# Optimization experiments

Measured on AMD Instinct MI355X. Metric: run time of the kernel, lower is better.

## Reference

```python
import jax, jax.numpy as jnp
import numpy as np

D_MODEL = 768
HEAD = 12
D_K = D_MODEL // HEAD


def setup_inputs() -> dict:
    key = jax.random.key(0)
    ks = jax.random.split(key, 9)
    s = 1.0 / np.sqrt(D_MODEL)
    return {
        "x": jax.random.normal(ks[0], (2, 4096, D_MODEL), dtype=jnp.float32),
        "Wq": jax.random.normal(ks[1], (D_MODEL, D_MODEL), dtype=jnp.float32) * s,
        "bq": jax.random.normal(ks[2], (D_MODEL,), dtype=jnp.float32) * 0.01,
        "Wk": jax.random.normal(ks[3], (D_MODEL, D_MODEL), dtype=jnp.float32) * s,
        "bk": jax.random.normal(ks[4], (D_MODEL,), dtype=jnp.float32) * 0.01,
        "Wv": jax.random.normal(ks[5], (D_MODEL, D_MODEL), dtype=jnp.float32) * s,
        "bv": jax.random.normal(ks[6], (D_MODEL,), dtype=jnp.float32) * 0.01,
        "Wo": jax.random.normal(ks[7], (D_MODEL, D_MODEL), dtype=jnp.float32) * s,
        "bo": jax.random.normal(ks[8], (D_MODEL,), dtype=jnp.float32) * 0.01,
    }


def reference(x, Wq, bq, Wk, bk, Wv, bv, Wo, bo):
    B, S, _ = x.shape
    # Linear projections, split into heads: [B, H, S, d_k]
    def proj(W, b):
        return (x @ W + b).reshape(B, S, HEAD, D_K).transpose(0, 2, 1, 3)
    Q, K, V = proj(Wq, bq), proj(Wk, bk), proj(Wv, bv)
    scale = 1.0 / jnp.sqrt(jnp.asarray(D_K, x.dtype))
    # [B, H, S, S] attention scores (materialized, as in the original module)
    scores = jnp.einsum('bhqd,bhkd->bhqk', Q, K) * scale
    probs = jax.nn.softmax(scores, axis=-1)  # dropout is identity in eval mode
    ctx = jnp.einsum('bhqk,bhkd->bhqd', probs, V)
    ctx = ctx.transpose(0, 2, 1, 3).reshape(B, S, D_MODEL)
    return ctx @ Wo + bo
```

## Files before the change

### kernel.cpp

```cpp
#include <hip/hip_runtime.h>

#define D_MODEL 768
#define S_LEN   4096
#define NHEAD   12
#define DK      64
#define TKA     64

typedef _Float16 f16;
typedef _Float16 f16x8 __attribute__((ext_vector_type(8)));
typedef _Float16 f16x4 __attribute__((ext_vector_type(4)));
typedef __fp16   fp16x2 __attribute__((ext_vector_type(2)));
typedef float    f32x4 __attribute__((ext_vector_type(4)));
typedef float    f32x2 __attribute__((ext_vector_type(2)));

#define MFMA16(a, b, c) __builtin_amdgcn_mfma_f32_16x16x32_f16(a, b, c, 0, 0, 0)

#define Q_PRESCALE 0.18033688f
#define SOFTMAX_C  11.54156036f

__device__ inline f16x8 ldf(const f16* p) {
    return *reinterpret_cast<const f16x8*>(p);
}

__device__ inline void gl2lds16(const f16* g, f16* l) {
    __builtin_amdgcn_global_load_lds(
        (const __attribute__((address_space(1))) void*)g,
        (__attribute__((address_space(3))) void*)l, 16, 0, 0);
}

__global__ __launch_bounds__(256) void cvt_x_kernel(const float* __restrict__ x,
                                                    f16* __restrict__ xb) {
    size_t i = ((size_t)blockIdx.x * 256 + threadIdx.x) * 4;
    float4 v = *reinterpret_cast<const float4*>(x + i);
    f16x4 o = { (f16)v.x, (f16)v.y, (f16)v.z, (f16)v.w };
    *reinterpret_cast<f16x4*>(xb + i) = o;
}

__global__ __launch_bounds__(256) void wtrans_kernel(const float* __restrict__ Wq,
                                                     const float* __restrict__ Wk,
                                                     const float* __restrict__ Wv,
                                                     const float* __restrict__ Wo,
                                                     f16* __restrict__ WT) {
    const int z = blockIdx.z;
    const float* in = (z == 0) ? Wq : (z == 1) ? Wk : (z == 2) ? Wv : Wo;
    f16* out = WT + (size_t)z * D_MODEL * D_MODEL;
    __shared__ float tile[32][33];
    const int tx = threadIdx.x, ty = threadIdx.y;
    const int n0 = blockIdx.x * 32, k0 = blockIdx.y * 32;
#pragma unroll
    for (int j = 0; j < 32; j += 8)
        tile[ty + j][tx] = in[(size_t)(k0 + ty + j) * D_MODEL + n0 + tx];
    __syncthreads();
#pragma unroll
    for (int j = 0; j < 32; j += 8)
        out[(size_t)(n0 + ty + j) * D_MODEL + k0 + tx] = (f16)tile[tx][ty + j];
}

__global__ __launch_bounds__(256, 3) void gemm_qkv_kernel(
        const f16* __restrict__ A, const f16* __restrict__ WT,
        const float* __restrict__ bq, const float* __restrict__ bk,
        const float* __restrict__ bv,
        f16* __restrict__ Qb, f16* __restrict__ Kb, f16* __restrict__ Vt) {
    __shared__ __align__(16) f16 asmem[3][128 * 32];
    __shared__ __align__(16) f16 bsmem[3][128 * 32];
    const int z = blockIdx.z;
    const f16* Bt = WT + (size_t)z * D_MODEL * D_MODEL;
    const float* bias = (z == 0) ? bq : (z == 1) ? bk : bv;
    const int w = threadIdx.x >> 6;
    const int lane = threadIdx.x & 63;
    const int ln = lane & 15, quad = lane >> 4;
    const int mb = blockIdx.x * 128;
    const int nb = blockIdx.y * 128;
    const int mloc = (w & 1) * 64, nloc = (w >> 1) * 64;
    const int l0 = w * 64 + lane;

    auto stage = [&](int buf, int kb) {
#pragma unroll
        for (int p = 0; p < 2; p++) {
            const int l = p * 256 + l0;
            gl2lds16(A + (size_t)(mb + (l >> 2)) * D_MODEL + kb + (l & 3) * 8,
                     &asmem[buf][(p * 256 + w * 64) * 8]);
        }
#pragma unroll
        for (int p = 0; p < 2; p++) {
            const int l = p * 256 + l0;
            gl2lds16(Bt + (size_t)(nb + (l >> 2)) * D_MODEL + kb + (l & 3) * 8,
                     &bsmem[buf][(p * 256 + w * 64) * 8]);
        }
    };

    f32x4 acc[4][4] = {};
    stage(0, 0);
    stage(1, 32);
    __syncthreads();

    const int NIT = D_MODEL / 32;
    int cb = 0, sb = 2;
    for (int it = 0; it < NIT; ++it) {
        f16x8 af[4], bf[4];
#pragma unroll
        for (int i = 0; i < 4; i++)
            af[i] = ldf(&asmem[cb][(mloc + i * 16 + ln) * 32 + quad * 8]);
#pragma unroll
        for (int t = 0; t < 4; t++)
            bf[t] = ldf(&bsmem[cb][(nloc + t * 16 + ln) * 32 + quad * 8]);
#pragma unroll
        for (int i = 0; i < 4; i++)
#pragma unroll
            for (int t = 0; t < 4; t++)
                acc[i][t] = MFMA16(af[i], bf[t], acc[i][t]);
        __syncthreads();
        if (it + 2 < NIT) stage(sb, (it + 2) * 32);
        cb = (cb == 2) ? 0 : cb + 1;
        sb = (sb == 2) ? 0 : sb + 1;
    }

#pragma unroll
    for (int t = 0; t < 4; t++) {
        const int n = nb + nloc + t * 16 + ln;
        const float bval = bias[n];
        const int h = n >> 6, d = n & 63;
#pragma unroll
        for (int i = 0; i < 4; i++) {
            const int m = mb + mloc + i * 16 + quad * 4;
            const int b = m >> 12, s = m & 4095;
            const int bh = b * NHEAD + h;
            if (z == 0) {
#pragma unroll
                for (int r = 0; r < 4; r++)
                    Qb[((size_t)bh * S_LEN + s + r) * DK + d] =
                        (f16)((acc[i][t][r] + bval) * Q_PRESCALE);
            } else if (z == 1) {
#pragma unroll
                for (int r = 0; r < 4; r++)
                    Kb[((size_t)bh * S_LEN + s + r) * DK + d] =
                        (f16)(acc[i][t][r] + bval);
            } else {
                f16x4 pk;
#pragma unroll
                for (int r = 0; r < 4; r++) pk[r] = (f16)(acc[i][t][r] + bval);
                *reinterpret_cast<f16x4*>(&Vt[((size_t)bh * DK + d) * S_LEN + s]) = pk;
            }
        }
    }
}

__global__ __launch_bounds__(256, 3) void attn_kernel(const f16* __restrict__ Qb,
                                                      const f16* __restrict__ Kb,
                                                      const f16* __restrict__ Vt,
                                                      f16* __restrict__ Ctx) {
    __shared__ __align__(16) f16 kbuf[3][TKA * DK];
    __shared__ __align__(16) f16 vbuf[3][DK * TKA];

    const int w = threadIdx.x >> 6;
    const int lane = threadIdx.x & 63;
    const int ln = lane & 15, quad = lane >> 4;

    const int blk = blockIdx.x;
    const int xcd = blk & 7, sidx = blk >> 3;
    const int bh = xcd * 3 + (sidx >> 5);
    const int qb = (sidx & 31) * 128;
    const int b = bh / NHEAD, h = bh % NHEAD;

    const f16* Kbh = Kb + (size_t)bh * S_LEN * DK;
    const f16* Vbh = Vt + (size_t)bh * DK * S_LEN;

    f16x8 aq[2][2];
#pragma unroll
    for (int i2 = 0; i2 < 2; i2++) {
        const f16* qp = Qb + ((size_t)bh * S_LEN + qb + w * 32 + i2 * 16 + ln) * DK;
        aq[i2][0] = ldf(qp + quad * 8);
        aq[i2][1] = ldf(qp + 32 + quad * 8);
    }

    int rS[2], ckS[2], cvS[2];
#pragma unroll
    for (int p = 0; p < 2; p++) {
        const int l = p * 256 + w * 64 + lane;
        const int r = l >> 3;
        rS[p]  = r;
        ckS[p] = ((l & 7) - r - (r >> 2)) & 7;
        cvS[p] = ((l & 7) - r - (r >> 3)) & 7;
    }

    auto stage = [&](int buf, int kk) {
#pragma unroll
        for (int p = 0; p < 2; p++)
            gl2lds16(Kbh + (size_t)(kk + rS[p]) * DK + ckS[p] * 8,
                     &kbuf[buf][(p * 256 + w * 64) * 8]);
#pragma unroll
        for (int p = 0; p < 2; p++)
            gl2lds16(Vbh + (size_t)rS[p] * S_LEN + kk + cvS[p] * 8,
                     &vbuf[buf][(p * 256 + w * 64) * 8]);
    };

    int koff[2][2][2];
#pragma unroll
    for (int kt = 0; kt < 2; kt++)
#pragma unroll
        for (int a = 0; a < 2; a++) {
            const int rr = kt * 32 + 8 * (ln >> 2) + 4 * a + (ln & 3);
            const int sw = rr + (rr >> 2);
            koff[kt][a][0] = rr * DK + (((quad + sw) & 7) * 8);
            koff[kt][a][1] = rr * DK + (((quad + 4 + sw) & 7) * 8);
        }
    int voff[4][2];
#pragma unroll
    for (int t = 0; t < 4; t++) {
        const int rr = t * 16 + ln;
        const int sw = rr + (rr >> 3);
#pragma unroll
        for (int kt = 0; kt < 2; kt++)
            voff[t][kt] = rr * TKA + (((quad + 4 * kt + sw) & 7) * 8);
    }

    const f32x4 cinit = { -SOFTMAX_C, -SOFTMAX_C, -SOFTMAX_C, -SOFTMAX_C };
    f32x4 acc[4][2] = {};
    f32x2 lsum2[2] = {};

    stage(0, 0);
    stage(1, TKA);
    __syncthreads();

    const int NIT = S_LEN / TKA;
    int cb = 0, sb = 2;
    for (int it = 0; it < NIT; ++it) {
        const f16* kb = kbuf[cb];
        const f16* vb = vbuf[cb];

        union { f16x8 v; fp16x2 h2[4]; } pb[2][2];

#pragma unroll
        for (int kt = 0; kt < 2; kt++) {
#pragma unroll
            for (int a = 0; a < 2; a++) {
                const f16x8 kf0 = ldf(kb + koff[kt][a][0]);
                const f16x8 kf1 = ldf(kb + koff[kt][a][1]);
#pragma unroll
                for (int i2 = 0; i2 < 2; i2++) {
                    f32x4 si = MFMA16(kf0, aq[i2][0], cinit);
                    si = MFMA16(kf1, aq[i2][1], si);
                    const float e0 = __builtin_amdgcn_exp2f(si[0]);
                    const float e1 = __builtin_amdgcn_exp2f(si[1]);
                    const float e2 = __builtin_amdgcn_exp2f(si[2]);
                    const float e3 = __builtin_amdgcn_exp2f(si[3]);
                    f32x2 ea = { e0, e1 };
                    f32x2 eb = { e2, e3 };
                    lsum2[i2] += ea + eb;
                    pb[kt][i2].h2[2 * a]     = __builtin_amdgcn_cvt_pkrtz(e0, e1);
                    pb[kt][i2].h2[2 * a + 1] = __builtin_amdgcn_cvt_pkrtz(e2, e3);
                }
            }
        }

        __builtin_amdgcn_s_setprio(1);
#pragma unroll
        for (int t = 0; t < 4; t++) {
#pragma unroll
            for (int kt = 0; kt < 2; kt++) {
                const f16x8 vf = ldf(vb + voff[t][kt]);
#pragma unroll
                for (int i2 = 0; i2 < 2; i2++)
                    acc[t][i2] = MFMA16(vf, pb[kt][i2].v, acc[t][i2]);
            }
        }
        __builtin_amdgcn_s_setprio(0);

        __syncthreads();
        if (it + 2 < NIT) stage(sb, (it + 2) * TKA);
        cb = (cb == 2) ? 0 : cb + 1;
        sb = (sb == 2) ? 0 : sb + 1;
    }

#pragma unroll
    for (int i2 = 0; i2 < 2; i2++) {
        float l = lsum2[i2][0] + lsum2[i2][1];
        l += __shfl_xor(l, 16, 64);
        l += __shfl_xor(l, 32, 64);
        const float rl = 1.0f / l;
        const int q = qb + w * 32 + i2 * 16 + ln;
        f16* cp = Ctx + ((size_t)b * S_LEN + q) * D_MODEL + h * DK + 4 * quad;
#pragma unroll
        for (int t = 0; t < 4; t++) {
            f16x4 pk;
#pragma unroll
            for (int r = 0; r < 4; r++) pk[r] = (f16)(acc[t][i2][r] * rl);
            *reinterpret_cast<f16x4*>(cp + t * 16) = pk;
        }
    }
}

__global__ __launch_bounds__(256, 3) void gemm_o_kernel(const f16* __restrict__ A,
                                                        const f16* __restrict__ Bt,
                                                        const float* __restrict__ bo,
                                                        float* __restrict__ out) {
    __shared__ __align__(16) f16 asmem[3][128 * 32];
    __shared__ __align__(16) f16 bsmem[3][128 * 32];
    const int w = threadIdx.x >> 6;
    const int lane = threadIdx.x & 63;
    const int ln = lane & 15, quad = lane >> 4;
    const int mb = blockIdx.x * 128;
    const int nb = blockIdx.y * 128;
    const int mloc = (w & 1) * 64, nloc = (w >> 1) * 64;
    const int l0 = w * 64 + lane;

    auto stage = [&](int buf, int kb) {
#pragma unroll
        for (int p = 0; p < 2; p++) {
            const int l = p * 256 + l0;
            gl2lds16(A + (size_t)(mb + (l >> 2)) * D_MODEL + kb + (l & 3) * 8,
                     &asmem[buf][(p * 256 + w * 64) * 8]);
        }
#pragma unroll
        for (int p = 0; p < 2; p++) {
            const int l = p * 256 + l0;
            gl2lds16(Bt + (size_t)(nb + (l >> 2)) * D_MODEL + kb + (l & 3) * 8,
                     &bsmem[buf][(p * 256 + w * 64) * 8]);
        }
    };

    f32x4 acc[4][4] = {};
    stage(0, 0);
    stage(1, 32);
    __syncthreads();

    const int NIT = D_MODEL / 32;
    int cb = 0, sb = 2;
    for (int it = 0; it < NIT; ++it) {
        f16x8 af[4], bf[4];
#pragma unroll
        for (int i = 0; i < 4; i++)
            af[i] = ldf(&asmem[cb][(mloc + i * 16 + ln) * 32 + quad * 8]);
#pragma unroll
        for (int t = 0; t < 4; t++)
            bf[t] = ldf(&bsmem[cb][(nloc + t * 16 + ln) * 32 + quad * 8]);
#pragma unroll
        for (int i = 0; i < 4; i++)
#pragma unroll
            for (int t = 0; t < 4; t++)
                acc[i][t] = MFMA16(af[i], bf[t], acc[i][t]);
        __syncthreads();
        if (it + 2 < NIT) stage(sb, (it + 2) * 32);
        cb = (cb == 2) ? 0 : cb + 1;
        sb = (sb == 2) ? 0 : sb + 1;
    }

#pragma unroll
    for (int t = 0; t < 4; t++) {
        const int n = nb + nloc + t * 16 + ln;
        const float bval = bo[n];
#pragma unroll
        for (int i = 0; i < 4; i++) {
            const int m = mb + mloc + i * 16 + quad * 4;
#pragma unroll
            for (int r = 0; r < 4; r++)
                out[(size_t)(m + r) * D_MODEL + n] = acc[i][t][r] + bval;
        }
    }
}

extern "C" void kernel_launch(void* const* d_in, const int* in_sizes, int n_in,
                              void* d_out, int out_size, void* d_ws, size_t ws_size,
                              hipStream_t stream) {
    const float* x  = (const float*)d_in[0];
    const float* Wq = (const float*)d_in[1];
    const float* bq = (const float*)d_in[2];
    const float* Wk = (const float*)d_in[3];
    const float* bk = (const float*)d_in[4];
    const float* Wv = (const float*)d_in[5];
    const float* bv = (const float*)d_in[6];
    const float* Wo = (const float*)d_in[7];
    const float* bo = (const float*)d_in[8];
    float* out = (float*)d_out;

    f16* ws = (f16*)d_ws;
    f16* Xb  = ws;
    f16* Ctx = ws;
    f16* WT  = ws + 6291456;
    f16* Qb  = ws + 8650752;
    f16* Kb  = ws + 14942208;
    f16* Vt  = ws + 21233664;

    cvt_x_kernel<<<6144, 256, 0, stream>>>(x, Xb);
    wtrans_kernel<<<dim3(24, 24, 4), dim3(32, 8), 0, stream>>>(Wq, Wk, Wv, Wo, WT);
    gemm_qkv_kernel<<<dim3(64, 6, 3), 256, 0, stream>>>(Xb, WT, bq, bk, bv, Qb, Kb, Vt);
    attn_kernel<<<768, 256, 0, stream>>>(Qb, Kb, Vt, Ctx);
    gemm_o_kernel<<<dim3(64, 6), 256, 0, stream>>>(Ctx, WT + (size_t)3 * D_MODEL * D_MODEL, bo, out);
}
```

Measured before the change: 272.8 us.

## Software-pipeline QK^T one tile ahead of softmax and PV in attention loop

```diff
diff --git a/kernel.cpp b/kernel.cpp
--- a/kernel.cpp
+++ b/kernel.cpp
@@ -217,45 +217,107 @@
     const f32x4 cinit = { -SOFTMAX_C, -SOFTMAX_C, -SOFTMAX_C, -SOFTMAX_C };
     f32x4 acc[4][2] = {};
     f32x2 lsum2[2] = {};
+    f32x4 siA[8], siB[8];
+
+    const int NIT = S_LEN / TKA;
 
     stage(0, 0);
     stage(1, TKA);
+    stage(2, 2 * TKA);
     __syncthreads();
 
-    const int NIT = S_LEN / TKA;
-    int cb = 0, sb = 2;
-    for (int it = 0; it < NIT; ++it) {
-        const f16* kb = kbuf[cb];
+#pragma unroll
+    for (int kt = 0; kt < 2; kt++)
+#pragma unroll
+        for (int a = 0; a < 2; a++) {
+            const f16x8 kf0 = ldf(kbuf[0] + koff[kt][a][0]);
+            const f16x8 kf1 = ldf(kbuf[0] + koff[kt][a][1]);
+#pragma unroll
+            for (int i2 = 0; i2 < 2; i2++) {
+                f32x4 s_ = MFMA16(kf0, aq[i2][0], cinit);
+                siA[(kt * 2 + a) * 2 + i2] = MFMA16(kf1, aq[i2][1], s_);
+            }
+        }
+
+    int cb = 0, cbn = 1;
+
+#define ATTN_STEP(SIA_, SIB_, itv)                                           \
+    {                                                                        \
+        const f16* kbn = kbuf[cbn];                                          \
+        const f16* vb  = vbuf[cb];                                           \
+        union { f16x8 v; fp16x2 h2[4]; } pb[2][2];                           \
+        _Pragma("unroll")                                                    \
+        for (int kt = 0; kt < 2; kt++) {                                     \
+            _Pragma("unroll")                                                \
+            for (int a = 0; a < 2; a++) {                                    \
+                const f16x8 kf0 = ldf(kbn + koff[kt][a][0]);                 \
+                const f16x8 kf1 = ldf(kbn + koff[kt][a][1]);                 \
+                _Pragma("unroll")                                            \
+                for (int i2 = 0; i2 < 2; i2++) {                             \
+                    const int g = (kt * 2 + a) * 2 + i2;                     \
+                    f32x4 s_ = MFMA16(kf0, aq[i2][0], cinit);                \
+                    const f32x4 sa = SIA_[g];                                \
+                    SIB_[g] = MFMA16(kf1, aq[i2][1], s_);                    \
+                    const float e0 = __builtin_amdgcn_exp2f(sa[0]);          \
+                    const float e1 = __builtin_amdgcn_exp2f(sa[1]);          \
+                    const float e2 = __builtin_amdgcn_exp2f(sa[2]);          \
+                    const float e3 = __builtin_amdgcn_exp2f(sa[3]);          \
+                    f32x2 ea = { e0, e1 };                                   \
+                    f32x2 eb = { e2, e3 };                                   \
+                    lsum2[i2] += ea + eb;                                    \
+                    pb[kt][i2].h2[2 * a]     = __builtin_amdgcn_cvt_pkrtz(e0, e1); \
+                    pb[kt][i2].h2[2 * a + 1] = __builtin_amdgcn_cvt_pkrtz(e2, e3); \
+                }                                                            \
+            }                                                                \
+        }                                                                    \
+        __builtin_amdgcn_s_setprio(1);                                       \
+        _Pragma("unroll")                                                    \
+        for (int t = 0; t < 4; t++) {                                        \
+            _Pragma("unroll")                                                \
+            for (int kt = 0; kt < 2; kt++) {                                 \
+                const f16x8 vf = ldf(vb + voff[t][kt]);                      \
+                _Pragma("unroll")                                            \
+                for (int i2 = 0; i2 < 2; i2++)                               \
+                    acc[t][i2] = MFMA16(vf, pb[kt][i2].v, acc[t][i2]);       \
+            }                                                                \
+        }                                                                    \
+        __builtin_amdgcn_s_setprio(0);                                       \
+        __syncthreads();                                                     \
+        if ((itv) + 3 < NIT) stage(cb, ((itv) + 3) * TKA);                   \
+        cb  = (cb  == 2) ? 0 : cb  + 1;                                      \
+        cbn = (cbn == 2) ? 0 : cbn + 1;                                      \
+    }
+
+#pragma unroll 1
+    for (int j = 0; j < 31; ++j) {
+        ATTN_STEP(siA, siB, 2 * j);
+        ATTN_STEP(siB, siA, 2 * j + 1);
+    }
+    ATTN_STEP(siA, siB, 62);
+#undef ATTN_STEP
+
+    {
         const f16* vb = vbuf[cb];
-
         union { f16x8 v; fp16x2 h2[4]; } pb[2][2];
-
-#pragma unroll
-        for (int kt = 0; kt < 2; kt++) {
-#pragma unroll
-            for (int a = 0; a < 2; a++) {
-                const f16x8 kf0 = ldf(kb + koff[kt][a][0]);
-                const f16x8 kf1 = ldf(kb + koff[kt][a][1]);
+#pragma unroll
+        for (int kt = 0; kt < 2; kt++)
+#pragma unroll
+            for (int a = 0; a < 2; a++)
 #pragma unroll
                 for (int i2 = 0; i2 < 2; i2++) {
-                    f32x4 si = MFMA16(kf0, aq[i2][0], cinit);
-                    si = MFMA16(kf1, aq[i2][1], si);
-                    const float e0 = __builtin_amdgcn_exp2f(si[0]);
-                    const float e1 = __builtin_amdgcn_exp2f(si[1]);
-                    const float e2 = __builtin_amdgcn_exp2f(si[2]);
-                    const float e3 = __builtin_amdgcn_exp2f(si[3]);
+                    const int g = (kt * 2 + a) * 2 + i2;
+                    const float e0 = __builtin_amdgcn_exp2f(siB[g][0]);
+                    const float e1 = __builtin_amdgcn_exp2f(siB[g][1]);
+                    const float e2 = __builtin_amdgcn_exp2f(siB[g][2]);
+                    const float e3 = __builtin_amdgcn_exp2f(siB[g][3]);
                     f32x2 ea = { e0, e1 };
                     f32x2 eb = { e2, e3 };
                     lsum2[i2] += ea + eb;
                     pb[kt][i2].h2[2 * a]     = __builtin_amdgcn_cvt_pkrtz(e0, e1);
                     pb[kt][i2].h2[2 * a + 1] = __builtin_amdgcn_cvt_pkrtz(e2, e3);
                 }
-            }
-        }
-
-        __builtin_amdgcn_s_setprio(1);
-#pragma unroll
-        for (int t = 0; t < 4; t++) {
+#pragma unroll
+        for (int t = 0; t < 4; t++)
 #pragma unroll
             for (int kt = 0; kt < 2; kt++) {
                 const f16x8 vf = ldf(vb + voff[t][kt]);
@@ -263,13 +325,6 @@
                 for (int i2 = 0; i2 < 2; i2++)
                     acc[t][i2] = MFMA16(vf, pb[kt][i2].v, acc[t][i2]);
             }
-        }
-        __builtin_amdgcn_s_setprio(0);
-
-        __syncthreads();
-        if (it + 2 < NIT) stage(sb, (it + 2) * TKA);
-        cb = (cb == 2) ? 0 : cb + 1;
-        sb = (sb == 2) ? 0 : sb + 1;
     }
 
 #pragma unroll
```

Measured after the change: 481.4 us. 76.5% more time.
